# Optimization experiments

Hardware: AMD Instinct MI355X
Metric: run time of the kernel (lower is better)

The kernel has to match this reference:

```python
import jax, jax.numpy as jnp
import numpy as np

N_ENT = 200000   # n_entities
N_NODES = 20000  # nodes in subgraph
N_EDGES = 320000 # avg degree 16
R = 40           # n_relations
B = 34           # num_bases (hard-coded in module)
D_IN = 128       # emb_dim_init
D_HID = 128      # hidden_dim
D_OUT = 128      # out_dim


def setup_inputs() -> dict:
    key = jax.random.key(0)
    ks = jax.random.split(key, 14)
    s = 0.05
    return {
        "node_index": jax.random.randint(ks[0], (N_NODES,), 0, N_ENT),
        "edge_index": jax.random.randint(ks[1], (2, N_EDGES), 0, N_NODES),
        "edge_type": jax.random.randint(ks[2], (N_EDGES,), 0, R),
        "node_frequency": jax.random.normal(ks[3], (N_NODES,), jnp.float32),
        "node_emb": jax.random.normal(ks[4], (N_ENT, D_IN), jnp.float32),
        "comp0": jax.random.normal(ks[5], (R, B), jnp.float32) * s,
        "bases0": jax.random.normal(ks[6], (B, D_IN, D_HID), jnp.float32) * s,
        "root0": jax.random.normal(ks[7], (D_IN, D_HID), jnp.float32) * s,
        "bias0": jnp.zeros((D_HID,), jnp.float32),
        "comp1": jax.random.normal(ks[8], (R, B), jnp.float32) * s,
        "bases1": jax.random.normal(ks[9], (B, D_HID, D_OUT), jnp.float32) * s,
        "root1": jax.random.normal(ks[10], (D_HID, D_OUT), jnp.float32) * s,
        "bias1": jnp.zeros((D_OUT,), jnp.float32),
    }


def _rgcn_conv(x, src, dst, etype, comp, bases, root, bias):
    """Basis-decomposed RGCNConv (PyG semantics: per-relation mean aggregation
    over incoming edges, plus root transform and bias)."""
    n = x.shape[0]
    # relation weights from basis decomposition: [R, in, out]
    W = jnp.einsum('rb,bio->rio', comp, bases)
    # transform all nodes by every relation weight: [R, N, out]
    h_all = jnp.einsum('ni,rio->rno', x, W)
    # gather per-edge message x[src] @ W[edge_type]: [E, out]
    msg = h_all[etype, src]
    # mean-aggregate per (dst node, relation) segment
    seg = dst * R + etype
    sums = jax.ops.segment_sum(msg, seg, num_segments=n * R)  # [N*R, out]
    cnt = jax.ops.segment_sum(jnp.ones((msg.shape[0],), x.dtype), seg,
                              num_segments=n * R)
    mean = sums / jnp.maximum(cnt, 1.0)[:, None]
    agg = mean.reshape(n, R, -1).sum(axis=1)  # sum over relations: [N, out]
    return agg + x @ root + bias


def reference(node_index, edge_index, edge_type, node_frequency, node_emb,
              comp0, bases0, root0, bias0, comp1, bases1, root1, bias1):
    # node_frequency is accepted but unused (matches original forward).
    x = node_emb[node_index]                      # [N, D_IN]
    src, dst = edge_index[0], edge_index[1]
    x = _rgcn_conv(x, src, dst, edge_type, comp0, bases0, root0, bias0)
    x = _rgcn_conv(x, src, dst, edge_type, comp1, bases1, root1, bias1)
    return x
```

## Files before the change

### kernel.cpp

```cpp
#include <hip/hip_runtime.h>

#define N_NODES  20000
#define N_EDGES  320000
#define R_REL    40
#define N_BASES  34
#define DIM      128
#define EB       128
#define P_PAD    (N_EDGES + R_REL * EB)
#define ROOT_PAD ((N_NODES + EB - 1) / EB * EB)
#define P2_MAX   (P_PAD + ROOT_PAD)
#define NE2      (N_EDGES + N_NODES)

typedef unsigned int uint;
typedef unsigned short ushort;
typedef __attribute__((ext_vector_type(8))) short short8;
typedef __attribute__((ext_vector_type(4))) float f32x4;

__device__ __forceinline__ ushort f2bf(float f) {
    uint u = __float_as_uint(f);
    return (ushort)((u + 0x7FFFu + ((u >> 16) & 1u)) >> 16);
}
__device__ __forceinline__ uint pk2bf(float a, float b) {
    return (uint)f2bf(a) | ((uint)f2bf(b) << 16);
}

__global__ void zero_kernel(int* __restrict__ p, int n) {
    int i = blockIdx.x * blockDim.x + threadIdx.x;
    if (i < n) p[i] = 0;
}

__global__ void fill_kernel(int* __restrict__ srcs, float* __restrict__ escale) {
    int i = blockIdx.x * blockDim.x + threadIdx.x;
    if (i < P2_MAX) { srcs[i] = -1; escale[i] = 0.0f; }
}

__global__ void count_kernel(const int* __restrict__ ei, const int* __restrict__ et,
                             int* __restrict__ c, int* __restrict__ h,
                             int* __restrict__ deg) {
    __shared__ int hloc[R_REL];
    int t = threadIdx.x;
    if (t < R_REL) hloc[t] = 0;
    __syncthreads();
    int e = blockIdx.x * blockDim.x + t;
    if (e < N_EDGES) {
        int dst = ei[N_EDGES + e];
        int r   = et[e];
        atomicAdd(&c[dst * R_REL + r], 1);
        atomicAdd(&deg[dst], 1);
        atomicAdd(&hloc[r], 1);
    }
    __syncthreads();
    if (t < R_REL && hloc[t]) atomicAdd(&h[t], hloc[t]);
}

__global__ void inv_kernel(const int* __restrict__ c, float* __restrict__ finv) {
    int i = blockIdx.x * blockDim.x + threadIdx.x;
    if (i < N_NODES * R_REL) {
        int v = c[i];
        finv[i] = 1.0f / (float)(v < 1 ? 1 : v);
    }
}

__global__ void scan_kernel(const int* __restrict__ h, int* __restrict__ off) {
    if (threadIdx.x == 0) {
        int acc = 0;
        off[0] = 0;
        for (int r = 0; r < R_REL; ++r) {
            acc += ((h[r] + EB - 1) / EB) * EB;
            off[r + 1] = acc;
        }
        off[R_REL + 1] = acc + ROOT_PAD;
    }
}

__global__ void scanptr_kernel(const int* __restrict__ deg, int* __restrict__ ptr) {
    __shared__ int part[256];
    const int CH = (N_NODES + 255) / 256;
    int t = threadIdx.x;
    int s = 0;
    for (int i = 0; i < CH; ++i) {
        int idx = t * CH + i;
        if (idx < N_NODES) s += deg[idx] + 1;
    }
    part[t] = s;
    __syncthreads();
    for (int d = 1; d < 256; d <<= 1) {
        int v = (t >= d) ? part[t - d] : 0;
        __syncthreads();
        part[t] += v;
        __syncthreads();
    }
    int base = (t > 0) ? part[t - 1] : 0;
    for (int i = 0; i < CH; ++i) {
        int idx = t * CH + i;
        if (idx < N_NODES) { ptr[idx] = base; base += deg[idx] + 1; }
    }
    if (t == 255) ptr[N_NODES] = NE2;
}

__global__ void place_kernel(const int* __restrict__ ei, const int* __restrict__ et,
                             const int* __restrict__ off, int* __restrict__ cur,
                             const float* __restrict__ finv,
                             const int* __restrict__ ptr, int* __restrict__ cur2,
                             int* __restrict__ srcs, float* __restrict__ escale,
                             int* __restrict__ ebyd) {
    __shared__ int hloc[R_REL];
    __shared__ int base[R_REL];
    int t = threadIdx.x;
    if (t < R_REL) hloc[t] = 0;
    __syncthreads();
    int e = blockIdx.x * blockDim.x + t;
    int r = 0, myrank = 0, src = 0, dst = 0;
    bool valid = (e < N_EDGES);
    if (valid) {
        r = et[e]; src = ei[e]; dst = ei[N_EDGES + e];
        myrank = atomicAdd(&hloc[r], 1);
    }
    __syncthreads();
    if (t < R_REL) base[t] = hloc[t] ? atomicAdd(&cur[t], hloc[t]) : 0;
    __syncthreads();
    if (valid) {
        int p = off[r] + base[r] + myrank;
        srcs[p]   = src;
        escale[p] = finv[dst * R_REL + r];
        int q = ptr[dst] + 1 + atomicAdd(&cur2[dst], 1);
        ebyd[q] = p;
    }
}

__global__ void rootplace_kernel(const int* __restrict__ off, const int* __restrict__ ptr,
                                 int* __restrict__ srcs, float* __restrict__ escale,
                                 int* __restrict__ ebyd) {
    int n = blockIdx.x * blockDim.x + threadIdx.x;
    if (n >= N_NODES) return;
    int p = off[R_REL] + n;
    srcs[p]   = n;
    escale[p] = 1.0f;
    ebyd[ptr[n]] = p;
}

__global__ void gather_bf16_kernel(const float* __restrict__ emb, const int* __restrict__ idx,
                                   ushort* __restrict__ xb) {
    int t = blockIdx.x * blockDim.x + threadIdx.x;
    int n = t >> 4, v = t & 15;
    const float4* s = (const float4*)(emb + (size_t)idx[n] * DIM + v * 8);
    float4 a = s[0], b = s[1];
    uint4 o;
    o.x = pk2bf(a.x, a.y); o.y = pk2bf(a.z, a.w);
    o.z = pk2bf(b.x, b.y); o.w = pk2bf(b.z, b.w);
    *(uint4*)(xb + (size_t)n * DIM + v * 8) = o;
}

__global__ void weights_kernel(const float* __restrict__ comp,
                               const float* __restrict__ bases,
                               float* __restrict__ Wf) {
    int t = blockIdx.x * blockDim.x + threadIdx.x;
    int col = t & (DIM - 1);
    int row = t >> 7;
    int r = row >> 7, i = row & (DIM - 1);
    float acc = 0.f;
    #pragma unroll
    for (int b = 0; b < N_BASES; ++b)
        acc += comp[r * N_BASES + b] * bases[((size_t)b * DIM + i) * DIM + col];
    Wf[t] = acc;
}

__global__ void transW_kernel(const float* __restrict__ Wf, const float* __restrict__ root,
                              ushort* __restrict__ Wt) {
    __shared__ float tile[32][33];
    int slot = blockIdx.x >> 4;
    int tb   = blockIdx.x & 15;
    int k0 = (tb >> 2) * 32, n0 = (tb & 3) * 32;
    const float* srcp = (slot < R_REL) ? (Wf + (size_t)slot * DIM * DIM) : root;
    int t = threadIdx.x;
    int tr = t >> 5, tc = t & 31;
    #pragma unroll
    for (int i = 0; i < 4; ++i)
        tile[tr + 8 * i][tc] = srcp[(size_t)(k0 + tr + 8 * i) * DIM + n0 + tc];
    __syncthreads();
    #pragma unroll
    for (int i = 0; i < 4; ++i) {
        int rr = tr + 8 * i;
        Wt[(size_t)slot * DIM * DIM + (size_t)(n0 + rr) * DIM + k0 + tc] = f2bf(tile[tc][rr]);
    }
}

__launch_bounds__(256)
__global__ void edge_mfma_kernel(const int* __restrict__ srcs, const float* __restrict__ escale,
                                 const int* __restrict__ off,
                                 const ushort* __restrict__ xb, const ushort* __restrict__ Wt,
                                 ushort* __restrict__ T) {
    __shared__ __align__(16) ushort Ws[DIM * DIM];
    __shared__ int soff[R_REL + 2];
    int t = threadIdx.x;
    if (t < R_REL + 2) soff[t] = off[t];
    __syncthreads();
    int e0 = blockIdx.x * EB;
    if (e0 >= soff[R_REL + 1]) return;
    int r = 0;
    while (e0 >= soff[r + 1]) ++r;

    const ushort* Wr = Wt + (size_t)r * DIM * DIM;
    #pragma unroll
    for (int i = 0; i < 8; ++i) {
        int idx = t + 256 * i;
        int row = idx >> 4, slot = idx & 15;
        uint4 v = *(const uint4*)(Wr + row * DIM + slot * 8);
        *(uint4*)(&Ws[row * DIM + ((slot ^ (row & 15)) * 8)]) = v;
    }
    __syncthreads();

    int wv = t >> 6;
    int l  = t & 63;
    int lr = l & 15;
    int lk = l >> 4;

    int er0 = e0 + wv * 32 + lr;
    int er1 = er0 + 16;
    int s0 = srcs[er0], s1 = srcs[er1];
    float esc0 = escale[er0], esc1 = escale[er1];
    const ushort* x0p = xb + (size_t)(s0 < 0 ? 0 : s0) * DIM;
    const ushort* x1p = xb + (size_t)(s1 < 0 ? 0 : s1) * DIM;

    short8 xf0[4], xf1[4];
    #pragma unroll
    for (int ks = 0; ks < 4; ++ks) {
        xf0[ks] = *(const short8*)(x0p + (ks * 4 + lk) * 8);
        xf1[ks] = *(const short8*)(x1p + (ks * 4 + lk) * 8);
    }

    f32x4 acc0[8] = {{0.f,0.f,0.f,0.f}}, acc1[8] = {{0.f,0.f,0.f,0.f}};
    #pragma unroll
    for (int mt = 0; mt < 8; ++mt) { acc0[mt] = (f32x4){0.f,0.f,0.f,0.f}; acc1[mt] = (f32x4){0.f,0.f,0.f,0.f}; }

    #pragma unroll
    for (int ks = 0; ks < 4; ++ks) {
        #pragma unroll
        for (int mt = 0; mt < 8; ++mt) {
            int row = mt * 16 + lr;
            int slot = (ks * 4 + lk) ^ lr;
            short8 wf = *(const short8*)(&Ws[row * DIM + slot * 8]);
            acc0[mt] = __builtin_amdgcn_mfma_f32_16x16x32_bf16(wf, xf0[ks], acc0[mt], 0, 0, 0);
            acc1[mt] = __builtin_amdgcn_mfma_f32_16x16x32_bf16(wf, xf1[ks], acc1[mt], 0, 0, 0);
        }
    }

    ushort* T0 = T + (size_t)er0 * DIM;
    ushort* T1 = T + (size_t)er1 * DIM;
    #pragma unroll
    for (int mt = 0; mt < 8; ++mt) {
        uint2 p0, p1;
        p0.x = pk2bf(acc0[mt][0] * esc0, acc0[mt][1] * esc0);
        p0.y = pk2bf(acc0[mt][2] * esc0, acc0[mt][3] * esc0);
        p1.x = pk2bf(acc1[mt][0] * esc1, acc1[mt][1] * esc1);
        p1.y = pk2bf(acc1[mt][2] * esc1, acc1[mt][3] * esc1);
        *(uint2*)(T0 + mt * 16 + lk * 4) = p0;
        *(uint2*)(T1 + mt * 16 + lk * 4) = p1;
    }
}

template<int OUT_BF16>
__global__ void aggregate_kernel(const int* __restrict__ ptr, const int* __restrict__ ebyd,
                                 const ushort* __restrict__ T, const float* __restrict__ bias,
                                 void* __restrict__ yout) {
    int n = blockIdx.x;
    int t = threadIdx.x;
    int s0 = ptr[n], s1 = ptr[n + 1];
    float a0 = bias[2 * t], a1 = bias[2 * t + 1];
    for (int q = s0; q < s1; ++q) {
        int p = ebyd[q];
        uint v = *(const uint*)(T + (size_t)p * DIM + 2 * t);
        a0 += __uint_as_float(v << 16);
        a1 += __uint_as_float(v & 0xFFFF0000u);
    }
    if (OUT_BF16) {
        ((uint*)yout)[n * 64 + t] = pk2bf(a0, a1);
    } else {
        ((float2*)yout)[n * 64 + t] = make_float2(a0, a1);
    }
}

extern "C" void kernel_launch(void* const* d_in, const int* in_sizes, int n_in,
                              void* d_out, int out_size, void* d_ws, size_t ws_size,
                              hipStream_t stream) {
    const int*   node_index = (const int*)d_in[0];
    const int*   edge_index = (const int*)d_in[1];
    const int*   edge_type  = (const int*)d_in[2];
    const float* node_emb   = (const float*)d_in[4];
    const float* comp0  = (const float*)d_in[5];
    const float* bases0 = (const float*)d_in[6];
    const float* root0  = (const float*)d_in[7];
    const float* bias0  = (const float*)d_in[8];
    const float* comp1  = (const float*)d_in[9];
    const float* bases1 = (const float*)d_in[10];
    const float* root1  = (const float*)d_in[11];
    const float* bias1  = (const float*)d_in[12];
    float* out = (float*)d_out;

    char* ws = (char*)d_ws;
    int*    c_cnt  = (int*)   (ws);
    float*  finv   = (float*) (ws +  3200000);
    float*  Wf     = (float*) (ws +  6400000);
    ushort* Wt     = (ushort*)(ws +  9021440);
    ushort* x0b    = (ushort*)(ws + 10364928);
    ushort* y0b    = (ushort*)(ws + 15484928);
    int*    srcs   = (int*)   (ws + 20604928);
    float*  escale = (float*) (ws + 21985792);
    int*    ebyd   = (int*)   (ws + 23366656);
    int*    meta   = (int*)   (ws + 24726656);
    int*    deg    = (int*)   (ws + 24727680);
    int*    cur2   = (int*)   (ws + 24807680);
    int*    ptr    = (int*)   (ws + 24887680);
    ushort* T      = (ushort*)(ws + 24967936);
    int* off = meta;
    int* h   = meta + 64;
    int* cur = meta + 128;

    zero_kernel<<<(N_NODES * R_REL + 255) / 256, 256, 0, stream>>>(c_cnt, N_NODES * R_REL);
    zero_kernel<<<(256 + 20000 + 20000 + 255) / 256, 256, 0, stream>>>(meta, 256 + 20000 + 20000);
    count_kernel<<<(N_EDGES + 255) / 256, 256, 0, stream>>>(edge_index, edge_type, c_cnt, h, deg);
    inv_kernel<<<(N_NODES * R_REL + 255) / 256, 256, 0, stream>>>(c_cnt, finv);
    scan_kernel<<<1, 64, 0, stream>>>(h, off);
    scanptr_kernel<<<1, 256, 0, stream>>>(deg, ptr);
    fill_kernel<<<(P2_MAX + 255) / 256, 256, 0, stream>>>(srcs, escale);
    place_kernel<<<(N_EDGES + 255) / 256, 256, 0, stream>>>(edge_index, edge_type, off, cur,
                                                            finv, ptr, cur2, srcs, escale, ebyd);
    rootplace_kernel<<<(N_NODES + 255) / 256, 256, 0, stream>>>(off, ptr, srcs, escale, ebyd);
    gather_bf16_kernel<<<N_NODES * 16 / 256, 256, 0, stream>>>(node_emb, node_index, x0b);

    const int wBlocks = R_REL * DIM * DIM / 256;
    const int tBlocks = (R_REL + 1) * 16;
    const int eBlocks = P2_MAX / EB;

    weights_kernel<<<wBlocks, 256, 0, stream>>>(comp0, bases0, Wf);
    transW_kernel<<<tBlocks, 256, 0, stream>>>(Wf, root0, Wt);
    edge_mfma_kernel<<<eBlocks, 256, 0, stream>>>(srcs, escale, off, x0b, Wt, T);
    aggregate_kernel<1><<<N_NODES, 64, 0, stream>>>(ptr, ebyd, T, bias0, y0b);

    weights_kernel<<<wBlocks, 256, 0, stream>>>(comp1, bases1, Wf);
    transW_kernel<<<tBlocks, 256, 0, stream>>>(Wf, root1, Wt);
    edge_mfma_kernel<<<eBlocks, 256, 0, stream>>>(srcs, escale, off, y0b, Wt, T);
    aggregate_kernel<0><<<N_NODES, 64, 0, stream>>>(ptr, ebyd, T, bias1, out);
}
```

Measured before the change: 290.6 us.

## Fuse setup kernels, pack edge metadata, write messages in dst order

```diff
diff --git a/kernel.cpp b/kernel.cpp
--- a/kernel.cpp
+++ b/kernel.cpp
@@ -24,14 +24,12 @@
     return (uint)f2bf(a) | ((uint)f2bf(b) << 16);
 }
 
-__global__ void zero_kernel(int* __restrict__ p, int n) {
+__global__ void init_kernel(int* __restrict__ c_cnt, int* __restrict__ meta_cur2_deg,
+                            uint4* __restrict__ esrc) {
     int i = blockIdx.x * blockDim.x + threadIdx.x;
-    if (i < n) p[i] = 0;
-}
-
-__global__ void fill_kernel(int* __restrict__ srcs, float* __restrict__ escale) {
-    int i = blockIdx.x * blockDim.x + threadIdx.x;
-    if (i < P2_MAX) { srcs[i] = -1; escale[i] = 0.0f; }
+    if (i < N_NODES * R_REL) c_cnt[i] = 0;
+    if (i < P2_MAX) esrc[i] = make_uint4((uint)-1, (uint)-1, 0u, 0u);
+    if (i < 256 + 2 * N_NODES) meta_cur2_deg[i] = 0;
 }
 
 __global__ void count_kernel(const int* __restrict__ ei, const int* __restrict__ et,
@@ -61,8 +59,31 @@
     }
 }
 
-__global__ void scan_kernel(const int* __restrict__ h, int* __restrict__ off) {
-    if (threadIdx.x == 0) {
+__global__ void scans_kernel(const int* __restrict__ deg, const int* __restrict__ h,
+                             int* __restrict__ ptr, int* __restrict__ off) {
+    __shared__ int part[256];
+    const int CHn = (N_NODES + 255) / 256;
+    int t = threadIdx.x;
+    int s = 0;
+    for (int i = 0; i < CHn; ++i) {
+        int idx = t * CHn + i;
+        if (idx < N_NODES) s += deg[idx] + 1;
+    }
+    part[t] = s;
+    __syncthreads();
+    for (int d = 1; d < 256; d <<= 1) {
+        int v = (t >= d) ? part[t - d] : 0;
+        __syncthreads();
+        part[t] += v;
+        __syncthreads();
+    }
+    int base = (t > 0) ? part[t - 1] : 0;
+    for (int i = 0; i < CHn; ++i) {
+        int idx = t * CHn + i;
+        if (idx < N_NODES) { ptr[idx] = base; base += deg[idx] + 1; }
+    }
+    if (t == 0) {
+        ptr[N_NODES] = NE2;
         int acc = 0;
         off[0] = 0;
         for (int r = 0; r < R_REL; ++r) {
@@ -73,37 +94,11 @@
     }
 }
 
-__global__ void scanptr_kernel(const int* __restrict__ deg, int* __restrict__ ptr) {
-    __shared__ int part[256];
-    const int CH = (N_NODES + 255) / 256;
-    int t = threadIdx.x;
-    int s = 0;
-    for (int i = 0; i < CH; ++i) {
-        int idx = t * CH + i;
-        if (idx < N_NODES) s += deg[idx] + 1;
-    }
-    part[t] = s;
-    __syncthreads();
-    for (int d = 1; d < 256; d <<= 1) {
-        int v = (t >= d) ? part[t - d] : 0;
-        __syncthreads();
-        part[t] += v;
-        __syncthreads();
-    }
-    int base = (t > 0) ? part[t - 1] : 0;
-    for (int i = 0; i < CH; ++i) {
-        int idx = t * CH + i;
-        if (idx < N_NODES) { ptr[idx] = base; base += deg[idx] + 1; }
-    }
-    if (t == 255) ptr[N_NODES] = NE2;
-}
-
 __global__ void place_kernel(const int* __restrict__ ei, const int* __restrict__ et,
                              const int* __restrict__ off, int* __restrict__ cur,
                              const float* __restrict__ finv,
                              const int* __restrict__ ptr, int* __restrict__ cur2,
-                             int* __restrict__ srcs, float* __restrict__ escale,
-                             int* __restrict__ ebyd) {
+                             uint4* __restrict__ esrc) {
     __shared__ int hloc[R_REL];
     __shared__ int base[R_REL];
     int t = threadIdx.x;
@@ -111,32 +106,23 @@
     __syncthreads();
     int e = blockIdx.x * blockDim.x + t;
     int r = 0, myrank = 0, src = 0, dst = 0;
-    bool valid = (e < N_EDGES);
-    if (valid) {
+    bool isEdge = (e < N_EDGES);
+    if (isEdge) {
         r = et[e]; src = ei[e]; dst = ei[N_EDGES + e];
         myrank = atomicAdd(&hloc[r], 1);
     }
     __syncthreads();
     if (t < R_REL) base[t] = hloc[t] ? atomicAdd(&cur[t], hloc[t]) : 0;
     __syncthreads();
-    if (valid) {
+    if (isEdge) {
         int p = off[r] + base[r] + myrank;
-        srcs[p]   = src;
-        escale[p] = finv[dst * R_REL + r];
         int q = ptr[dst] + 1 + atomicAdd(&cur2[dst], 1);
-        ebyd[q] = p;
-    }
-}
-
-__global__ void rootplace_kernel(const int* __restrict__ off, const int* __restrict__ ptr,
-                                 int* __restrict__ srcs, float* __restrict__ escale,
-                                 int* __restrict__ ebyd) {
-    int n = blockIdx.x * blockDim.x + threadIdx.x;
-    if (n >= N_NODES) return;
-    int p = off[R_REL] + n;
-    srcs[p]   = n;
-    escale[p] = 1.0f;
-    ebyd[ptr[n]] = p;
+        esrc[p] = make_uint4((uint)src, (uint)q,
+                             __float_as_uint(finv[dst * R_REL + r]), 0u);
+    } else if (e < N_EDGES + N_NODES) {
+        int n = e - N_EDGES;
+        esrc[off[R_REL] + n] = make_uint4((uint)n, (uint)ptr[n], 0x3f800000u, 0u);
+    }
 }
 
 __global__ void gather_bf16_kernel(const float* __restrict__ emb, const int* __restrict__ idx,
@@ -151,32 +137,33 @@
     *(uint4*)(xb + (size_t)n * DIM + v * 8) = o;
 }
 
-__global__ void weights_kernel(const float* __restrict__ comp,
-                               const float* __restrict__ bases,
-                               float* __restrict__ Wf) {
-    int t = blockIdx.x * blockDim.x + threadIdx.x;
-    int col = t & (DIM - 1);
-    int row = t >> 7;
-    int r = row >> 7, i = row & (DIM - 1);
-    float acc = 0.f;
-    #pragma unroll
-    for (int b = 0; b < N_BASES; ++b)
-        acc += comp[r * N_BASES + b] * bases[((size_t)b * DIM + i) * DIM + col];
-    Wf[t] = acc;
-}
-
-__global__ void transW_kernel(const float* __restrict__ Wf, const float* __restrict__ root,
-                              ushort* __restrict__ Wt) {
+__global__ void wtrans_kernel(const float* __restrict__ comp, const float* __restrict__ bases,
+                              const float* __restrict__ root, ushort* __restrict__ Wt) {
     __shared__ float tile[32][33];
+    __shared__ float scomp[N_BASES];
     int slot = blockIdx.x >> 4;
     int tb   = blockIdx.x & 15;
     int k0 = (tb >> 2) * 32, n0 = (tb & 3) * 32;
-    const float* srcp = (slot < R_REL) ? (Wf + (size_t)slot * DIM * DIM) : root;
-    int t = threadIdx.x;
-    int tr = t >> 5, tc = t & 31;
-    #pragma unroll
-    for (int i = 0; i < 4; ++i)
-        tile[tr + 8 * i][tc] = srcp[(size_t)(k0 + tr + 8 * i) * DIM + n0 + tc];
+    int t = threadIdx.x, tr = t >> 5, tc = t & 31;
+    if (slot < R_REL) {
+        if (t < N_BASES) scomp[t] = comp[slot * N_BASES + t];
+        __syncthreads();
+        #pragma unroll
+        for (int i = 0; i < 4; ++i) {
+            int kk = tr + 8 * i;
+            float acc = 0.f;
+            #pragma unroll
+            for (int b = 0; b < N_BASES; ++b)
+                acc += scomp[b] * bases[((size_t)b * DIM + k0 + kk) * DIM + n0 + tc];
+            tile[kk][tc] = acc;
+        }
+    } else {
+        #pragma unroll
+        for (int i = 0; i < 4; ++i) {
+            int kk = tr + 8 * i;
+            tile[kk][tc] = root[(size_t)(k0 + kk) * DIM + n0 + tc];
+        }
+    }
     __syncthreads();
     #pragma unroll
     for (int i = 0; i < 4; ++i) {
@@ -186,8 +173,7 @@
 }
 
 __launch_bounds__(256)
-__global__ void edge_mfma_kernel(const int* __restrict__ srcs, const float* __restrict__ escale,
-                                 const int* __restrict__ off,
+__global__ void edge_mfma_kernel(const uint4* __restrict__ esrc, const int* __restrict__ off,
                                  const ushort* __restrict__ xb, const ushort* __restrict__ Wt,
                                  ushort* __restrict__ T) {
     __shared__ __align__(16) ushort Ws[DIM * DIM];
@@ -217,8 +203,10 @@
 
     int er0 = e0 + wv * 32 + lr;
     int er1 = er0 + 16;
-    int s0 = srcs[er0], s1 = srcs[er1];
-    float esc0 = escale[er0], esc1 = escale[er1];
+    uint4 es0 = esrc[er0], es1 = esrc[er1];
+    int s0 = (int)es0.x, q0 = (int)es0.y;
+    int s1 = (int)es1.x, q1 = (int)es1.y;
+    float esc0 = __uint_as_float(es0.z), esc1 = __uint_as_float(es1.z);
     const ushort* x0p = xb + (size_t)(s0 < 0 ? 0 : s0) * DIM;
     const ushort* x1p = xb + (size_t)(s1 < 0 ? 0 : s1) * DIM;
 
@@ -229,7 +217,7 @@
         xf1[ks] = *(const short8*)(x1p + (ks * 4 + lk) * 8);
     }
 
-    f32x4 acc0[8] = {{0.f,0.f,0.f,0.f}}, acc1[8] = {{0.f,0.f,0.f,0.f}};
+    f32x4 acc0[8], acc1[8];
     #pragma unroll
     for (int mt = 0; mt < 8; ++mt) { acc0[mt] = (f32x4){0.f,0.f,0.f,0.f}; acc1[mt] = (f32x4){0.f,0.f,0.f,0.f}; }
 
@@ -245,31 +233,34 @@
         }
     }
 
-    ushort* T0 = T + (size_t)er0 * DIM;
-    ushort* T1 = T + (size_t)er1 * DIM;
+    ushort* T0 = T + (size_t)q0 * DIM;
+    ushort* T1 = T + (size_t)q1 * DIM;
     #pragma unroll
     for (int mt = 0; mt < 8; ++mt) {
-        uint2 p0, p1;
-        p0.x = pk2bf(acc0[mt][0] * esc0, acc0[mt][1] * esc0);
-        p0.y = pk2bf(acc0[mt][2] * esc0, acc0[mt][3] * esc0);
-        p1.x = pk2bf(acc1[mt][0] * esc1, acc1[mt][1] * esc1);
-        p1.y = pk2bf(acc1[mt][2] * esc1, acc1[mt][3] * esc1);
-        *(uint2*)(T0 + mt * 16 + lk * 4) = p0;
-        *(uint2*)(T1 + mt * 16 + lk * 4) = p1;
+        if (q0 >= 0) {
+            uint2 p0;
+            p0.x = pk2bf(acc0[mt][0] * esc0, acc0[mt][1] * esc0);
+            p0.y = pk2bf(acc0[mt][2] * esc0, acc0[mt][3] * esc0);
+            *(uint2*)(T0 + mt * 16 + lk * 4) = p0;
+        }
+        if (q1 >= 0) {
+            uint2 p1;
+            p1.x = pk2bf(acc1[mt][0] * esc1, acc1[mt][1] * esc1);
+            p1.y = pk2bf(acc1[mt][2] * esc1, acc1[mt][3] * esc1);
+            *(uint2*)(T1 + mt * 16 + lk * 4) = p1;
+        }
     }
 }
 
 template<int OUT_BF16>
-__global__ void aggregate_kernel(const int* __restrict__ ptr, const int* __restrict__ ebyd,
-                                 const ushort* __restrict__ T, const float* __restrict__ bias,
-                                 void* __restrict__ yout) {
+__global__ void aggregate_kernel(const int* __restrict__ ptr, const ushort* __restrict__ T,
+                                 const float* __restrict__ bias, void* __restrict__ yout) {
     int n = blockIdx.x;
     int t = threadIdx.x;
     int s0 = ptr[n], s1 = ptr[n + 1];
     float a0 = bias[2 * t], a1 = bias[2 * t + 1];
     for (int q = s0; q < s1; ++q) {
-        int p = ebyd[q];
-        uint v = *(const uint*)(T + (size_t)p * DIM + 2 * t);
+        uint v = *(const uint*)(T + (size_t)q * DIM + 2 * t);
         a0 += __uint_as_float(v << 16);
         a1 += __uint_as_float(v & 0xFFFF0000u);
     }
@@ -300,45 +291,35 @@
     char* ws = (char*)d_ws;
     int*    c_cnt  = (int*)   (ws);
     float*  finv   = (float*) (ws +  3200000);
-    float*  Wf     = (float*) (ws +  6400000);
-    ushort* Wt     = (ushort*)(ws +  9021440);
-    ushort* x0b    = (ushort*)(ws + 10364928);
-    ushort* y0b    = (ushort*)(ws + 15484928);
-    int*    srcs   = (int*)   (ws + 20604928);
-    float*  escale = (float*) (ws + 21985792);
-    int*    ebyd   = (int*)   (ws + 23366656);
-    int*    meta   = (int*)   (ws + 24726656);
-    int*    deg    = (int*)   (ws + 24727680);
-    int*    cur2   = (int*)   (ws + 24807680);
-    int*    ptr    = (int*)   (ws + 24887680);
-    ushort* T      = (ushort*)(ws + 24967936);
+    ushort* Wt     = (ushort*)(ws +  6400000);
+    ushort* x0b    = (ushort*)(ws +  7743488);
+    ushort* y0b    = (ushort*)(ws + 12863488);
+    uint4*  esrc   = (uint4*) (ws + 17983488);
+    int*    meta   = (int*)   (ws + 23506944);
+    int*    cur2   = (int*)   (ws + 23507968);
+    int*    deg    = (int*)   (ws + 23587968);
+    int*    ptr    = (int*)   (ws + 23667968);
+    ushort* T      = (ushort*)(ws + 23748480);
     int* off = meta;
     int* h   = meta + 64;
     int* cur = meta + 128;
 
-    zero_kernel<<<(N_NODES * R_REL + 255) / 256, 256, 0, stream>>>(c_cnt, N_NODES * R_REL);
-    zero_kernel<<<(256 + 20000 + 20000 + 255) / 256, 256, 0, stream>>>(meta, 256 + 20000 + 20000);
+    init_kernel<<<(N_NODES * R_REL + 255) / 256, 256, 0, stream>>>(c_cnt, meta, esrc);
     count_kernel<<<(N_EDGES + 255) / 256, 256, 0, stream>>>(edge_index, edge_type, c_cnt, h, deg);
     inv_kernel<<<(N_NODES * R_REL + 255) / 256, 256, 0, stream>>>(c_cnt, finv);
-    scan_kernel<<<1, 64, 0, stream>>>(h, off);
-    scanptr_kernel<<<1, 256, 0, stream>>>(deg, ptr);
-    fill_kernel<<<(P2_MAX + 255) / 256, 256, 0, stream>>>(srcs, escale);
-    place_kernel<<<(N_EDGES + 255) / 256, 256, 0, stream>>>(edge_index, edge_type, off, cur,
-                                                            finv, ptr, cur2, srcs, escale, ebyd);
-    rootplace_kernel<<<(N_NODES + 255) / 256, 256, 0, stream>>>(off, ptr, srcs, escale, ebyd);
+    scans_kernel<<<1, 256, 0, stream>>>(deg, h, ptr, off);
+    place_kernel<<<(N_EDGES + N_NODES + 255) / 256, 256, 0, stream>>>(
+        edge_index, edge_type, off, cur, finv, ptr, cur2, esrc);
     gather_bf16_kernel<<<N_NODES * 16 / 256, 256, 0, stream>>>(node_emb, node_index, x0b);
 
-    const int wBlocks = R_REL * DIM * DIM / 256;
-    const int tBlocks = (R_REL + 1) * 16;
-    const int eBlocks = P2_MAX / EB;
-
-    weights_kernel<<<wBlocks, 256, 0, stream>>>(comp0, bases0, Wf);
-    transW_kernel<<<tBlocks, 256, 0, stream>>>(Wf, root0, Wt);
-    edge_mfma_kernel<<<eBlocks, 256, 0, stream>>>(srcs, escale, off, x0b, Wt, T);
-    aggregate_kernel<1><<<N_NODES, 64, 0, stream>>>(ptr, ebyd, T, bias0, y0b);
-
-    weights_kernel<<<wBlocks, 256, 0, stream>>>(comp1, bases1, Wf);
-    transW_kernel<<<tBlocks, 256, 0, stream>>>(Wf, root1, Wt);
-    edge_mfma_kernel<<<eBlocks, 256, 0, stream>>>(srcs, escale, off, y0b, Wt, T);
-    aggregate_kernel<0><<<N_NODES, 64, 0, stream>>>(ptr, ebyd, T, bias1, out);
-}
+    const int wtBlocks = (R_REL + 1) * 16;
+    const int eBlocks  = P2_MAX / EB;
+
+    wtrans_kernel<<<wtBlocks, 256, 0, stream>>>(comp0, bases0, root0, Wt);
+    edge_mfma_kernel<<<eBlocks, 256, 0, stream>>>(esrc, off, x0b, Wt, T);
+    aggregate_kernel<1><<<N_NODES, 64, 0, stream>>>(ptr, T, bias0, y0b);
+
+    wtrans_kernel<<<wtBlocks, 256, 0, stream>>>(comp1, bases1, root1, Wt);
+    edge_mfma_kernel<<<eBlocks, 256, 0, stream>>>(esrc, off, y0b, Wt, T);
+    aggregate_kernel<0><<<N_NODES, 64, 0, stream>>>(ptr, T, bias1, out);
+}
```

New measurement: 285.2 us. Within noise of the previous version (-1.8%).
